# Kernel optimization log

Measured on AMD Instinct MI355X. Metric: run time of the kernel, lower is better.

## Reference

```python
import jax, jax.numpy as jnp
import numpy as np

TINY = 1e-6
SGNUM = 12

def _ln(x, g, b):
    m = jnp.mean(x, -1, keepdims=True)
    v = jnp.mean((x - m) ** 2, -1, keepdims=True)
    return (x - m) * jax.lax.rsqrt(v + 1e-5) * g + b

def _mean_var(x, w):
    # weighted mean/variance over the view dim (-2), keepdim
    mean = jnp.sum(x * w, -2, keepdims=True)
    var = jnp.sum(w * (x - mean) ** 2, -2, keepdims=True)
    return mean, var

def setup_inputs():
    BN, H, W, N = 1, 128, 128, 8
    CTX, PF, PH, HD, MH, FH = 61, 32, 64, 32, 256, 128
    D = CTX + 3 + PF  # 96
    key = jax.random.key(0)
    ks = iter(jax.random.split(key, 64))
    def rnm(shape):
        return jax.random.normal(next(ks), shape, jnp.float32)
    def pw(shape):
        return jax.random.normal(next(ks), shape, jnp.float32) * 0.02
    inp = dict(
        rgb=jax.random.uniform(next(ks), (BN, H, W, N, 3), jnp.float32),
        featmaps_dense=rnm((BN, H, W, 1, CTX)),
        view_dir=rnm((BN, H, W, N, 3)),
        proj_err=rnm((BN, H, W, N, 1)),
        normal=rnm((BN, H, W, 1, 3)),
        DL=rnm((BN, H, W, SGNUM * 7)),
        # pbr_mlp: LN(7) -> Lin(7,PH) ELU -> Lin(PH,PH) ELU -> Lin(PH,PH) ELU -> Lin(PH,PF)
        pbr_ln_g=jnp.ones((7,), jnp.float32), pbr_ln_b=jnp.zeros((7,), jnp.float32),
        pbr_w1=pw((7, PH)), pbr_b1=jnp.zeros((PH,), jnp.float32),
        pbr_w2=pw((PH, PH)), pbr_b2=jnp.zeros((PH,), jnp.float32),
        pbr_w3=pw((PH, PH)), pbr_b3=jnp.zeros((PH,), jnp.float32),
        pbr_w4=pw((PH, PF)), pbr_b4=jnp.zeros((PF,), jnp.float32),
        # transformer block 1
        tv1_ln_g=jnp.ones((D,), jnp.float32), tv1_ln_b=jnp.zeros((D,), jnp.float32),
        tv1_w=pw((D, HD)),
        to1_w=pw((3 * HD, D)), to1_b=jnp.zeros((D,), jnp.float32),
        n1_ln_g=jnp.ones((D,), jnp.float32), n1_ln_b=jnp.zeros((D,), jnp.float32),
        n1_w1=pw((D, MH)), n1_b1=jnp.zeros((MH,), jnp.float32),
        n1_w2=pw((MH, D)), n1_b2=jnp.zeros((D,), jnp.float32),
        # transformer block 2
        tv2_ln_g=jnp.ones((D,), jnp.float32), tv2_ln_b=jnp.zeros((D,), jnp.float32),
        tv2_w=pw((D, HD)),
        to2_w=pw((3 * HD, D)), to2_b=jnp.zeros((D,), jnp.float32),
        n2_ln_g=jnp.ones((D,), jnp.float32), n2_ln_b=jnp.zeros((D,), jnp.float32),
        n2_w1=pw((D, MH)), n2_b1=jnp.zeros((MH,), jnp.float32),
        n2_w2=pw((MH, D)), n2_b2=jnp.zeros((D,), jnp.float32),
        # mlp_brdf
        brdf_ln_g=jnp.ones((D,), jnp.float32), brdf_ln_b=jnp.zeros((D,), jnp.float32),
        brdf_w1=pw((D, FH)), brdf_b1=jnp.zeros((FH,), jnp.float32),
        brdf_w2=pw((FH, FH)), brdf_b2=jnp.zeros((FH,), jnp.float32),
    )
    return inp

def reference(rgb, featmaps_dense, view_dir, proj_err, normal, DL,
              pbr_ln_g, pbr_ln_b, pbr_w1, pbr_b1, pbr_w2, pbr_b2, pbr_w3, pbr_b3, pbr_w4, pbr_b4,
              tv1_ln_g, tv1_ln_b, tv1_w, to1_w, to1_b,
              n1_ln_g, n1_ln_b, n1_w1, n1_b1, n1_w2, n1_b2,
              tv2_ln_g, tv2_ln_b, tv2_w, to2_w, to2_b,
              n2_ln_g, n2_ln_b, n2_w1, n2_b1, n2_w2, n2_b2,
              brdf_ln_g, brdf_ln_b, brdf_w1, brdf_b1, brdf_w2, brdf_b2):
    bn, h, w, n, _ = rgb.shape
    # view weights from reprojection error
    wgt = -jnp.minimum(jnp.log10(jnp.abs(proj_err) + TINY), 0.0)
    wgt = wgt / (jnp.sum(wgt, -2, keepdims=True) + TINY)  # [bn,h,w,n,1]
    DL6 = DL.reshape(bn, h, w, 1, SGNUM, 7)
    dl_dir = DL6[..., :3]
    DLdotN = jnp.sum(dl_dir * normal[:, :, :, :, None, :], -1, keepdims=True)  # [bn,h,w,1,SG,1]
    hdotV = (jnp.sum(dl_dir * view_dir[:, :, :, :, None, :], -1, keepdims=True) + 1.0) * 0.5  # [bn,h,w,n,SG,1]
    fresnel = jnp.exp2((-5.55472 * hdotV - 6.98316) * hdotV)
    VdotN = jnp.sum(view_dir * normal, -1, keepdims=True)[..., None, :]  # [bn,h,w,n,1,1]
    part = jnp.broadcast_to(jnp.concatenate([DLdotN, DL6[..., 3:]], -1), (bn, h, w, n, SGNUM, 5))
    VdotN = jnp.broadcast_to(VdotN, (bn, h, w, n, SGNUM, 1))
    pbr = jnp.concatenate([part, fresnel, VdotN], -1)  # [bn,h,w,n,SG,7]
    y = _ln(pbr, pbr_ln_g, pbr_ln_b)
    y = jax.nn.elu(y @ pbr_w1 + pbr_b1)
    y = jax.nn.elu(y @ pbr_w2 + pbr_b2)
    y = jax.nn.elu(y @ pbr_w3 + pbr_b3)
    pbr_feature = jnp.sum(y @ pbr_w4 + pbr_b4, -2)  # sum over SGNum -> [bn,h,w,n,PF]
    fm = jnp.broadcast_to(featmaps_dense, (bn, h, w, n, featmaps_dense.shape[-1]))
    x_input = jnp.concatenate([rgb, fm, pbr_feature], -1)  # [bn,h,w,n,D]
    # transformer block 1
    v = _ln(x_input, tv1_ln_g, tv1_ln_b) @ tv1_w  # [bn,h,w,n,HD]
    mean, var = _mean_var(v, wgt)
    mv = jnp.broadcast_to(jnp.concatenate([mean, var], -1), v.shape[:-1] + (2 * v.shape[-1],))
    x = jnp.concatenate([v, mv], -1) @ to1_w + to1_b + x_input
    x = jax.nn.gelu(_ln(x, n1_ln_g, n1_ln_b) @ n1_w1 + n1_b1, approximate=False) @ n1_w2 + n1_b2 + x_input
    # transformer block 2 (collapses view dim)
    v = _ln(x, tv2_ln_g, tv2_ln_b) @ tv2_w
    mean, var = _mean_var(v, wgt)
    x = (jnp.concatenate([v[..., :1, :], mean, var], -1) @ to2_w + to2_b)[..., 0, :]
    x = x + x_input[..., 0, :]
    x = jax.nn.gelu(_ln(x, n2_ln_g, n2_ln_b) @ n2_w1 + n2_b1, approximate=False) @ n2_w2 + n2_b2 + x_input[..., 0, :]
    brdf = jax.nn.gelu(_ln(x, brdf_ln_g, brdf_ln_b) @ brdf_w1 + brdf_b1, approximate=False) @ brdf_w2 + brdf_b2
    return brdf  # [bn,h,w,final_hidden]
```

## Files before the change

### kernel.cpp

```cpp
#include <hip/hip_runtime.h>
#include <math.h>


#define NPIX 16384

__device__ __forceinline__ float elu_f(float x){ return x > 0.f ? x : (__expf(x) - 1.f); }
__device__ __forceinline__ float gelu_f(float x){ return 0.5f*x*(1.f + erff(x*0.70710678118654752f)); }

__device__ __forceinline__ void fma4(float4& a, float s, const float4 w){
  a.x = fmaf(s, w.x, a.x); a.y = fmaf(s, w.y, a.y);
  a.z = fmaf(s, w.z, a.z); a.w = fmaf(s, w.w, a.w);
}
__device__ __forceinline__ float4 elu4f(float4 a){
  return make_float4(elu_f(a.x), elu_f(a.y), elu_f(a.z), elu_f(a.w));
}

#define NTA 768
#define NBA (NPIX/2)

constexpr int AYA   = 0;
constexpr int AYB   = 13056;
constexpr int AWB   = 26112;
constexpr int AXL   = 30208;
constexpr int ABIAS = 31744;
constexpr int ATOT  = 31968;

template<int K, int SI, bool DOELU>
__device__ __forceinline__ void mmA64(const float* __restrict__ Xin,
                                      const float* __restrict__ WB,
                                      const float* __restrict__ bias,
                                      float* __restrict__ Yout, int t)
{
  const int rq = t >> 4, c4 = t & 15;
  const float* x0 = Xin + (4*rq+0)*SI;
  const float* x1 = Xin + (4*rq+1)*SI;
  const float* x2 = Xin + (4*rq+2)*SI;
  const float* x3 = Xin + (4*rq+3)*SI;
  const float4* __restrict__ W4 = (const float4*)WB;
  const float4 b = ((const float4*)bias)[c4];
  float4 a0=b, a1=b, a2=b, a3=b;
  #pragma unroll
  for (int k2 = 0; k2 < K/2; ++k2){
    const float2 xa = *(const float2*)(x0 + 2*k2);
    const float2 xb = *(const float2*)(x1 + 2*k2);
    const float2 xc = *(const float2*)(x2 + 2*k2);
    const float2 xd = *(const float2*)(x3 + 2*k2);
    const float4 wA = W4[(2*k2)*16 + c4];
    const float4 wB = W4[(2*k2+1)*16 + c4];
    fma4(a0, xa.x, wA); fma4(a0, xa.y, wB);
    fma4(a1, xb.x, wA); fma4(a1, xb.y, wB);
    fma4(a2, xc.x, wA); fma4(a2, xc.y, wB);
    fma4(a3, xd.x, wA); fma4(a3, xd.y, wB);
  }
  if (DOELU){ a0 = elu4f(a0); a1 = elu4f(a1); a2 = elu4f(a2); a3 = elu4f(a3); }
  *(float4*)(Yout + (4*rq+0)*68 + 4*c4) = a0;
  *(float4*)(Yout + (4*rq+1)*68 + 4*c4) = a1;
  *(float4*)(Yout + (4*rq+2)*68 + 4*c4) = a2;
  *(float4*)(Yout + (4*rq+3)*68 + 4*c4) = a3;
}

__device__ __forceinline__ void mmA32(const float* __restrict__ Xin,
                                      const float* __restrict__ WB,
                                      const float* __restrict__ bias,
                                      float* __restrict__ F, int t)
{
  const int rq = t >> 4, c2 = t & 15;
  const float* x0 = Xin + (4*rq+0)*68;
  const float* x1 = Xin + (4*rq+1)*68;
  const float* x2 = Xin + (4*rq+2)*68;
  const float* x3 = Xin + (4*rq+3)*68;
  const float2* __restrict__ W2 = (const float2*)WB;
  const float2 b = ((const float2*)bias)[c2];
  float2 a0=b, a1=b, a2=b, a3=b;
  #pragma unroll
  for (int k2 = 0; k2 < 32; ++k2){
    const float2 xa = *(const float2*)(x0 + 2*k2);
    const float2 xb = *(const float2*)(x1 + 2*k2);
    const float2 xc = *(const float2*)(x2 + 2*k2);
    const float2 xd = *(const float2*)(x3 + 2*k2);
    const float2 wA = W2[(2*k2)*16 + c2];
    const float2 wB = W2[(2*k2+1)*16 + c2];
    a0.x = fmaf(xa.x, wA.x, a0.x); a0.y = fmaf(xa.x, wA.y, a0.y);
    a0.x = fmaf(xa.y, wB.x, a0.x); a0.y = fmaf(xa.y, wB.y, a0.y);
    a1.x = fmaf(xb.x, wA.x, a1.x); a1.y = fmaf(xb.x, wA.y, a1.y);
    a1.x = fmaf(xb.y, wB.x, a1.x); a1.y = fmaf(xb.y, wB.y, a1.y);
    a2.x = fmaf(xc.x, wA.x, a2.x); a2.y = fmaf(xc.x, wA.y, a2.y);
    a2.x = fmaf(xc.y, wB.x, a2.x); a2.y = fmaf(xc.y, wB.y, a2.y);
    a3.x = fmaf(xd.x, wA.x, a3.x); a3.y = fmaf(xd.x, wA.y, a3.y);
    a3.x = fmaf(xd.y, wB.x, a3.x); a3.y = fmaf(xd.y, wB.y, a3.y);
  }
  *(float2*)(F + (4*rq+0)*34 + 2*c2) = a0;
  *(float2*)(F + (4*rq+1)*34 + 2*c2) = a1;
  *(float2*)(F + (4*rq+2)*34 + 2*c2) = a2;
  *(float2*)(F + (4*rq+3)*34 + 2*c2) = a3;
}

__global__ __launch_bounds__(NTA)
void mva_phaseA(const float* __restrict__ view_dir, const float* __restrict__ normal,
                const float* __restrict__ DL,
                const float* __restrict__ ln_g, const float* __restrict__ ln_b,
                const float* __restrict__ w1, const float* __restrict__ b1,
                const float* __restrict__ w2, const float* __restrict__ b2,
                const float* __restrict__ w3, const float* __restrict__ b3,
                const float* __restrict__ w4, const float* __restrict__ b4,
                float* __restrict__ feat)
{
  __shared__ __align__(16) float smem[ATOT];
  const int t = threadIdx.x;
  const int bpx0 = blockIdx.x*2;
  float4* WB4 = (float4*)(smem + AWB);

  {
    const float4* s = (const float4*)w1;
    for (int i = t; i < 128; i += NTA){
      const int k = i >> 4, c4 = i & 15;
      WB4[i] = (k < 7) ? s[k*16 + c4] : make_float4(0.f,0.f,0.f,0.f);
    }
    float4* d = (float4*)(smem+ABIAS);
    if (t >= 256 && t < 272)      d[t-256]      = ((const float4*)b1)[t-256];
    else if (t >= 272 && t < 288) d[16 + t-272] = ((const float4*)b2)[t-272];
    else if (t >= 288 && t < 304) d[32 + t-288] = ((const float4*)b3)[t-288];
    else if (t >= 304 && t < 312) d[48 + t-304] = ((const float4*)b4)[t-304];
  }
  if (t < 192){
    const int pl = t / 96, rr = t - pl*96;
    const int sg = rr >> 3, view = rr & 7;
    const int px = bpx0 + pl;
    const float nm0 = normal[px*3+0], nm1 = normal[px*3+1], nm2 = normal[px*3+2];
    const float* vd = view_dir + (px*8 + view)*3;
    const float vd0 = vd[0], vd1 = vd[1], vd2 = vd[2];
    const float* dl = DL + px*84 + sg*7;
    const float d0=dl[0], d1=dl[1], d2=dl[2], d3=dl[3], d4=dl[4], d5=dl[5], d6=dl[6];

    const float DLdotN = d0*nm0 + d1*nm1 + d2*nm2;
    const float hv     = (d0*vd0 + d1*vd1 + d2*vd2 + 1.f)*0.5f;
    const float fres   = exp2f((-5.55472f*hv - 6.98316f)*hv);
    const float VdotN  = vd0*nm0 + vd1*nm1 + vd2*nm2;

    const float x0 = DLdotN, x1 = d3, x2 = d4, x3 = d5, x4 = d6, x5 = fres, x6 = VdotN;
    const float m  = (x0+x1+x2+x3+x4+x5+x6)*(1.f/7.f);
    float q, var = 0.f;
    q = x0-m; var += q*q; q = x1-m; var += q*q; q = x2-m; var += q*q;
    q = x3-m; var += q*q; q = x4-m; var += q*q; q = x5-m; var += q*q;
    q = x6-m; var += q*q;
    const float rs = rsqrtf(var*(1.f/7.f) + 1e-5f);
    float* xl = smem + AXL + t*8;
    xl[0] = (x0-m)*rs*ln_g[0] + ln_b[0];
    xl[1] = (x1-m)*rs*ln_g[1] + ln_b[1];
    xl[2] = (x2-m)*rs*ln_g[2] + ln_b[2];
    xl[3] = (x3-m)*rs*ln_g[3] + ln_b[3];
    xl[4] = (x4-m)*rs*ln_g[4] + ln_b[4];
    xl[5] = (x5-m)*rs*ln_g[5] + ln_b[5];
    xl[6] = (x6-m)*rs*ln_g[6] + ln_b[6];
    xl[7] = 0.f;
  }
  __syncthreads();

  float4 p0 = ((const float4*)w2)[t];
  float4 p1 = (t < 256) ? ((const float4*)w2)[t + 768] : make_float4(0.f,0.f,0.f,0.f);
  mmA64<8,8,true>(smem+AXL, smem+AWB, smem+ABIAS+0, smem+AYA, t);
  __syncthreads();
  WB4[t] = p0; if (t < 256) WB4[t + 768] = p1;
  __syncthreads();

  p0 = ((const float4*)w3)[t];
  p1 = (t < 256) ? ((const float4*)w3)[t + 768] : make_float4(0.f,0.f,0.f,0.f);
  mmA64<64,68,true>(smem+AYA, smem+AWB, smem+ABIAS+64, smem+AYB, t);
  __syncthreads();
  WB4[t] = p0; if (t < 256) WB4[t + 768] = p1;
  __syncthreads();

  p0 = (t < 512) ? ((const float4*)w4)[t] : make_float4(0.f,0.f,0.f,0.f);
  mmA64<64,68,true>(smem+AYB, smem+AWB, smem+ABIAS+128, smem+AYA, t);
  __syncthreads();
  if (t < 512) WB4[t] = p0;
  __syncthreads();

  mmA32(smem+AYA, smem+AWB, smem+ABIAS+192, smem+AYB, t);
  __syncthreads();

  if (t < 512){
    const int pl = t >> 8, idx = t & 255;
    const int v = idx >> 5, c = idx & 31;
    float s = 0.f;
    #pragma unroll
    for (int sg = 0; sg < 12; ++sg) s += smem[AYB + (pl*96 + sg*8 + v)*34 + c];
    feat[(size_t)(bpx0 + pl)*256 + idx] = s;
  }
}

#define NTB 512

template<int KK, int CC, int LDWG>
__device__ __forceinline__ void stageW(const float* __restrict__ Wg, int c4off,
                                       float* __restrict__ wbuf, int t)
{
  constexpr int C4 = CC/4;
  constexpr int N4 = KK*C4;
  const float4* __restrict__ s = (const float4*)Wg;
  float4* d = (float4*)wbuf;
  for (int i = t; i < N4; i += NTB){
    const int k = i / C4, c4 = i - k*C4;
    d[i] = s[k*(LDWG/4) + c4off + c4];
  }
}

#define PFSLOT(Wg, KK, CC, LDWG, C4OFF, SLOT, PFV) { \
  const int _i = t + (SLOT)*512; \
  if ((KK)*((CC)/4) > (SLOT)*512 && _i < (KK)*((CC)/4)){ \
    const int _k = _i/((CC)/4), _c = _i - _k*((CC)/4); \
    PFV = ((const float4*)(Wg))[_k*((LDWG)/4) + (C4OFF) + _c]; } }

#define PFLOADG(Wg, KK, CC, LDWG, C4OFF) \
  PFSLOT(Wg,KK,CC,LDWG,C4OFF,0,pf0) PFSLOT(Wg,KK,CC,LDWG,C4OFF,1,pf1) \
  PFSLOT(Wg,KK,CC,LDWG,C4OFF,2,pf2) PFSLOT(Wg,KK,CC,LDWG,C4OFF,3,pf3) \
  PFSLOT(Wg,KK,CC,LDWG,C4OFF,4,pf4) PFSLOT(Wg,KK,CC,LDWG,C4OFF,5,pf5)

#define PFWR(N4, SLOT, PFV) { if ((N4) > (SLOT)*512 && t + (SLOT)*512 < (N4)) WB4[t+(SLOT)*512] = PFV; }
#define PFWRITE(KK, CC) { \
  PFWR((KK)*((CC)/4),0,pf0) PFWR((KK)*((CC)/4),1,pf1) PFWR((KK)*((CC)/4),2,pf2) \
  PFWR((KK)*((CC)/4),3,pf3) PFWR((KK)*((CC)/4),4,pf4) PFWR((KK)*((CC)/4),5,pf5) }

__device__ __forceinline__ void ln32s(const float* __restrict__ in, int Si,
                                      float* __restrict__ out, int So,
                                      const float* __restrict__ g, const float* __restrict__ b,
                                      int t)
{
  if (t < 256){
    const int r = t >> 3, l8 = t & 7;
    const float* row = in + r*Si;
    float vals[12]; int cols[12];
    float s1 = 0.f, s2 = 0.f;
    #pragma unroll
    for (int i = 0; i < 12; ++i){
      int c = l8 + 8*i + 8*(r & 7); if (c >= 96) c -= 96;
      float a = row[c];
      cols[i] = c; vals[i] = a; s1 += a; s2 += a*a;
    }
    s1 += __shfl_xor(s1, 1); s2 += __shfl_xor(s2, 1);
    s1 += __shfl_xor(s1, 2); s2 += __shfl_xor(s2, 2);
    s1 += __shfl_xor(s1, 4); s2 += __shfl_xor(s2, 4);
    float mean = s1*(1.f/96.f);
    float var  = s2*(1.f/96.f) - mean*mean;
    float rsd = rsqrtf(var + 1e-5f);
    float* orow = out + r*So;
    #pragma unroll
    for (int i = 0; i < 12; ++i){
      int c = cols[i];
      orow[c] = (vals[i]-mean)*rsd*g[c] + b[c];
    }
  }
}

template<int K, int C, int LDW, bool GELU, bool HASB, bool RES, bool ACC>
__device__ __forceinline__ void mmR32(const float* __restrict__ inb, int S,
                                      const float* __restrict__ Wl, const float* __restrict__ bg,
                                      float* __restrict__ outb, int So,
                                      const float* __restrict__ residb, int Sr, int t)
{
  constexpr int C4 = C/4;
  const float4* __restrict__ W4 = (const float4*)Wl;
  for (int gi = t; gi < C4*16; gi += NTB){
    const int rp = gi & 15, c4 = gi >> 4;
    const float2* x0 = (const float2*)(inb + (2*rp)*S);
    const float2* x1 = (const float2*)(inb + (2*rp+1)*S);
    float4 a0 = HASB ? ((const float4*)bg)[c4] : make_float4(0.f,0.f,0.f,0.f);
    float4 a1 = a0;
    #pragma unroll 8
    for (int k2 = 0; k2 < K/2; ++k2){
      float2 xa = x0[k2], xb = x1[k2];
      float4 wA = W4[(2*k2)*(LDW/4) + c4];
      float4 wB = W4[(2*k2+1)*(LDW/4) + c4];
      fma4(a0, xa.x, wA); fma4(a0, xa.y, wB);
      fma4(a1, xb.x, wA); fma4(a1, xb.y, wB);
    }
    if (GELU){
      a0.x=gelu_f(a0.x); a0.y=gelu_f(a0.y); a0.z=gelu_f(a0.z); a0.w=gelu_f(a0.w);
      a1.x=gelu_f(a1.x); a1.y=gelu_f(a1.y); a1.z=gelu_f(a1.z); a1.w=gelu_f(a1.w);
    }
    if (RES){
      const float* r0 = residb + (2*rp)*Sr + 4*c4;
      const float* r1 = residb + (2*rp+1)*Sr + 4*c4;
      a0.x += r0[0]; a0.y += r0[1]; a0.z += r0[2]; a0.w += r0[3];
      a1.x += r1[0]; a1.y += r1[1]; a1.z += r1[2]; a1.w += r1[3];
    }
    float* o0 = outb + (2*rp)*So + 4*c4;
    float* o1 = outb + (2*rp+1)*So + 4*c4;
    if (ACC){
      a0.x += o0[0]; a0.y += o0[1]; a0.z += o0[2]; a0.w += o0[3];
      a1.x += o1[0]; a1.y += o1[1]; a1.z += o1[2]; a1.w += o1[3];
    }
    o0[0]=a0.x; o0[1]=a0.y; o0[2]=a0.z; o0[3]=a0.w;
    o1[0]=a1.x; o1[1]=a1.y; o1[2]=a1.z; o1[3]=a1.w;
  }
}

#define NBB1 (NPIX/4)
constexpr int BXIN  = 0;
constexpr int BXCUR = 3264;
constexpr int BXLN  = 6528;
constexpr int BHID  = 9792;
constexpr int BVB   = 14080;
constexpr int BMEAN = 15296;
constexpr int BVAR  = 15424;
constexpr int BWGT  = 15552;
constexpr int BWBUF = 15584;
constexpr int B1TOT = 27872;

__global__ __launch_bounds__(NTB)
void mva_phaseB1(const float* __restrict__ rgb, const float* __restrict__ fm,
                 const float* __restrict__ proj_err, float* __restrict__ ws,
                 const float* __restrict__ tv1_ln_g, const float* __restrict__ tv1_ln_b,
                 const float* __restrict__ tv1_w,
                 const float* __restrict__ to1_w, const float* __restrict__ to1_b,
                 const float* __restrict__ n1_ln_g, const float* __restrict__ n1_ln_b,
                 const float* __restrict__ n1_w1, const float* __restrict__ n1_b1,
                 const float* __restrict__ n1_w2, const float* __restrict__ n1_b2,
                 const float* __restrict__ tv2_ln_g, const float* __restrict__ tv2_ln_b,
                 const float* __restrict__ tv2_w)
{
  __shared__ __align__(16) float smem[B1TOT];
  const int t = threadIdx.x;
  const int bpx0 = blockIdx.x*4;
  float* WB = smem + BWBUF;
  float4* WB4 = (float4*)WB;
  float4 pf0 = make_float4(0,0,0,0), pf1 = pf0, pf2 = pf0, pf3 = pf0, pf4 = pf0, pf5 = pf0;

  for (int u = t; u < 2048; u += NTB){
    const int r = u >> 6, k = u & 63;
    const int pl = r >> 3, v = r & 7;
    float val = (k < 3) ? rgb[((bpx0+pl)*8 + v)*3 + k]
                        : fm[(bpx0+pl)*61 + (k-3)];
    smem[BXIN + r*102 + k] = val;
  }
  for (int u = t; u < 1024; u += NTB){
    const int r = u >> 5, c = u & 31;
    smem[BXIN + r*102 + 64 + c] = ws[(size_t)blockIdx.x*1024 + u];
  }
  if (t < 32){
    float pe = proj_err[(bpx0 + (t>>3))*8 + (t&7)];
    float wraw = fmaxf(-log10f(fabsf(pe) + 1e-6f), 0.f);
    float s = wraw;
    s += __shfl_xor(s, 1); s += __shfl_xor(s, 2); s += __shfl_xor(s, 4);
    smem[BWGT + t] = wraw / (s + 1e-6f);
  }
  stageW<96,32,32>(tv1_w, 0, WB, t);
  __syncthreads();

  ln32s(smem+BXIN, 102, smem+BXLN, 102, tv1_ln_g, tv1_ln_b, t);
  PFLOADG(to1_w, 96,96,96, 0)
  __syncthreads();
  mmR32<96,32,32,false,false,false,false>(smem+BXLN, 102, WB, nullptr, smem+BVB, 38, nullptr, 0, t);
  __syncthreads();
  if (t < 128){
    const int pl = t >> 5, c = t & 31;
    const float* wn = smem + BWGT + pl*8;
    float m = 0.f;
    #pragma unroll
    for (int v = 0; v < 8; ++v) m += wn[v]*smem[BVB + (pl*8+v)*38 + c];
    float vv = 0.f;
    #pragma unroll
    for (int v = 0; v < 8; ++v){ float d = smem[BVB + (pl*8+v)*38 + c] - m; vv += wn[v]*d*d; }
    smem[BMEAN + pl*32 + c] = m;
    smem[BVAR  + pl*32 + c] = vv;
  }
  PFWRITE(96,96)
  __syncthreads();
  for (int u = t; u < 3072; u += NTB){
    const int r = u & 31, c = u >> 5;
    const int pl = r >> 3;
    float val = (c < 32) ? smem[BVB + r*38 + c]
              : (c < 64) ? smem[BMEAN + pl*32 + (c-32)]
                         : smem[BVAR + pl*32 + (c-64)];
    smem[BXLN + r*102 + c] = val;
  }
  __syncthreads();
  PFLOADG(n1_w1, 96,128,256, 0)
  mmR32<96,96,96,false,true,true,false>(smem+BXLN, 102, WB, to1_b, smem+BXCUR, 102, smem+BXIN, 102, t);
  __syncthreads();
  ln32s(smem+BXCUR, 102, smem+BXLN, 102, n1_ln_g, n1_ln_b, t);
  PFWRITE(96,128)
  __syncthreads();
  PFLOADG(n1_w2, 128,96,96, 0)
  mmR32<96,128,128,true,true,false,false>(smem+BXLN, 102, WB, n1_b1, smem+BHID, 134, nullptr, 0, t);
  __syncthreads();
  PFWRITE(128,96)
  __syncthreads();
  PFLOADG(n1_w1, 96,128,256, 32)
  mmR32<128,96,96,false,false,false,false>(smem+BHID, 134, WB, nullptr, smem+BXCUR, 102, nullptr, 0, t);
  __syncthreads();
  PFWRITE(96,128)
  __syncthreads();
  PFLOADG(n1_w2 + 128*96, 128,96,96, 0)
  mmR32<96,128,128,true,true,false,false>(smem+BXLN, 102, WB, n1_b1 + 128, smem+BHID, 134, nullptr, 0, t);
  __syncthreads();
  PFWRITE(128,96)
  __syncthreads();
  PFLOADG(tv2_w, 96,32,32, 0)
  mmR32<128,96,96,false,true,true,true>(smem+BHID, 134, WB, n1_b2, smem+BXCUR, 102, smem+BXIN, 102, t);
  __syncthreads();
  ln32s(smem+BXCUR, 102, smem+BXLN, 102, tv2_ln_g, tv2_ln_b, t);
  PFWRITE(96,32)
  __syncthreads();
  mmR32<96,32,32,false,false,false,false>(smem+BXLN, 102, WB, nullptr, smem+BVB, 38, nullptr, 0, t);
  __syncthreads();
  if (t < 128){
    const int pl = t >> 5, c = t & 31;
    const float* wn = smem + BWGT + pl*8;
    float m = 0.f;
    #pragma unroll
    for (int v = 0; v < 8; ++v) m += wn[v]*smem[BVB + (pl*8+v)*38 + c];
    float vv = 0.f;
    #pragma unroll
    for (int v = 0; v < 8; ++v){ float d = smem[BVB + (pl*8+v)*38 + c] - m; vv += wn[v]*d*d; }
    smem[BMEAN + pl*32 + c] = m;
    smem[BVAR  + pl*32 + c] = vv;
  }
  __syncthreads();
  if (t < 384){
    const int pl = t / 96, c = t - pl*96;
    float val = (c < 32) ? smem[BVB + (pl*8)*38 + c]
              : (c < 64) ? smem[BMEAN + pl*32 + (c-32)]
                         : smem[BVAR + pl*32 + (c-64)];
    ws[(size_t)blockIdx.x*1024 + pl*256 + 96 + c] = val;
  }
}

#define NBB2 (NPIX/32)
constexpr int CXLN  = 0;
constexpr int CXIN  = 3264;
constexpr int CXS   = 6528;
constexpr int CTMP  = 9792;
constexpr int CHID  = 13056;
constexpr int CWBUF = 17344;
constexpr int B2TOT = 29632;

__global__ __launch_bounds__(NTB)
void mva_phaseB2(const float* __restrict__ rgb, const float* __restrict__ fm,
                 const float* __restrict__ ws,
                 const float* __restrict__ to2_w, const float* __restrict__ to2_b,
                 const float* __restrict__ n2_ln_g, const float* __restrict__ n2_ln_b,
                 const float* __restrict__ n2_w1, const float* __restrict__ n2_b1,
                 const float* __restrict__ n2_w2, const float* __restrict__ n2_b2,
                 const float* __restrict__ brdf_ln_g, const float* __restrict__ brdf_ln_b,
                 const float* __restrict__ brdf_w1, const float* __restrict__ brdf_b1,
                 const float* __restrict__ brdf_w2, const float* __restrict__ brdf_b2,
                 float* __restrict__ out)
{
  __shared__ __align__(16) float smem[B2TOT];
  const int t = threadIdx.x;
  const int bpx0 = blockIdx.x*32;
  float* WB = smem + CWBUF;
  float4* WB4 = (float4*)WB;
  float4 pf0 = make_float4(0,0,0,0), pf1 = pf0, pf2 = pf0, pf3 = pf0, pf4 = pf0, pf5 = pf0;

  for (int u = t; u < 3072; u += NTB){
    const int r = u / 96, c = u - r*96;
    const int px = bpx0 + r;
    const size_t ab = (size_t)px*256;
    smem[CXLN + r*102 + c] = ws[ab + 96 + c];
    float xv = (c < 3)  ? rgb[((size_t)px*8)*3 + c]
             : (c < 64) ? fm[(size_t)px*61 + (c-3)]
                        : ws[ab + (c-64)];
    smem[CXIN + r*102 + c] = xv;
  }
  stageW<96,96,96>(to2_w, 0, WB, t);
  __syncthreads();

  PFLOADG(n2_w1, 96,128,256, 0)
  mmR32<96,96,96,false,true,true,false>(smem+CXLN, 102, WB, to2_b, smem+CXS, 102, smem+CXIN, 102, t);
  __syncthreads();
  ln32s(smem+CXS, 102, smem+CXLN, 102, n2_ln_g, n2_ln_b, t);
  PFWRITE(96,128)
  __syncthreads();
  PFLOADG(n2_w2, 128,96,96, 0)
  mmR32<96,128,128,true,true,false,false>(smem+CXLN, 102, WB, n2_b1, smem+CHID, 134, nullptr, 0, t);
  __syncthreads();
  PFWRITE(128,96)
  __syncthreads();
  PFLOADG(n2_w1, 96,128,256, 32)
  mmR32<128,96,96,false,false,false,false>(smem+CHID, 134, WB, nullptr, smem+CTMP, 102, nullptr, 0, t);
  __syncthreads();
  PFWRITE(96,128)
  __syncthreads();
  PFLOADG(n2_w2 + 128*96, 128,96,96, 0)
  mmR32<96,128,128,true,true,false,false>(smem+CXLN, 102, WB, n2_b1 + 128, smem+CHID, 134, nullptr, 0, t);
  __syncthreads();
  PFWRITE(128,96)
  __syncthreads();
  PFLOADG(brdf_w1, 96,128,128, 0)
  mmR32<128,96,96,false,true,true,true>(smem+CHID, 134, WB, n2_b2, smem+CTMP, 102, smem+CXIN, 102, t);
  __syncthreads();
  ln32s(smem+CTMP, 102, smem+CXLN, 102, brdf_ln_g, brdf_ln_b, t);
  PFWRITE(96,128)
  __syncthreads();
  PFLOADG(brdf_w2, 128,64,128, 0)
  mmR32<96,128,128,true,true,false,false>(smem+CXLN, 102, WB, brdf_b1, smem+CHID, 134, nullptr, 0, t);
  __syncthreads();
  PFWRITE(128,64)
  __syncthreads();
  float* outp = out + (size_t)bpx0*128;
  PFLOADG(brdf_w2, 128,64,128, 16)
  mmR32<128,64,64,false,true,false,false>(smem+CHID, 134, WB, brdf_b2, outp, 128, nullptr, 0, t);
  __syncthreads();
  PFWRITE(128,64)
  __syncthreads();
  mmR32<128,64,64,false,true,false,false>(smem+CHID, 134, WB, brdf_b2 + 64, outp + 64, 128, nullptr, 0, t);
}

extern "C" void kernel_launch(void* const* d_in, const int* in_sizes, int n_in,
                              void* d_out, int out_size, void* d_ws, size_t ws_size,
                              hipStream_t stream)
{
  (void)in_sizes; (void)n_in; (void)ws_size; (void)out_size;
  int i = 0;
  const float* rgb      = (const float*)d_in[i++];
  const float* fm       = (const float*)d_in[i++];
  const float* view_dir = (const float*)d_in[i++];
  const float* proj_err = (const float*)d_in[i++];
  const float* normal   = (const float*)d_in[i++];
  const float* DL       = (const float*)d_in[i++];
  const float* pbr_ln_g = (const float*)d_in[i++];
  const float* pbr_ln_b = (const float*)d_in[i++];
  const float* pbr_w1   = (const float*)d_in[i++];
  const float* pbr_b1   = (const float*)d_in[i++];
  const float* pbr_w2   = (const float*)d_in[i++];
  const float* pbr_b2   = (const float*)d_in[i++];
  const float* pbr_w3   = (const float*)d_in[i++];
  const float* pbr_b3   = (const float*)d_in[i++];
  const float* pbr_w4   = (const float*)d_in[i++];
  const float* pbr_b4   = (const float*)d_in[i++];
  const float* tv1_ln_g = (const float*)d_in[i++];
  const float* tv1_ln_b = (const float*)d_in[i++];
  const float* tv1_w    = (const float*)d_in[i++];
  const float* to1_w    = (const float*)d_in[i++];
  const float* to1_b    = (const float*)d_in[i++];
  const float* n1_ln_g  = (const float*)d_in[i++];
  const float* n1_ln_b  = (const float*)d_in[i++];
  const float* n1_w1    = (const float*)d_in[i++];
  const float* n1_b1    = (const float*)d_in[i++];
  const float* n1_w2    = (const float*)d_in[i++];
  const float* n1_b2    = (const float*)d_in[i++];
  const float* tv2_ln_g = (const float*)d_in[i++];
  const float* tv2_ln_b = (const float*)d_in[i++];
  const float* tv2_w    = (const float*)d_in[i++];
  const float* to2_w    = (const float*)d_in[i++];
  const float* to2_b    = (const float*)d_in[i++];
  const float* n2_ln_g  = (const float*)d_in[i++];
  const float* n2_ln_b  = (const float*)d_in[i++];
  const float* n2_w1    = (const float*)d_in[i++];
  const float* n2_b1    = (const float*)d_in[i++];
  const float* n2_w2    = (const float*)d_in[i++];
  const float* n2_b2    = (const float*)d_in[i++];
  const float* brdf_ln_g= (const float*)d_in[i++];
  const float* brdf_ln_b= (const float*)d_in[i++];
  const float* brdf_w1  = (const float*)d_in[i++];
  const float* brdf_b1  = (const float*)d_in[i++];
  const float* brdf_w2  = (const float*)d_in[i++];
  const float* brdf_b2  = (const float*)d_in[i++];

  float* ws = (float*)d_ws;

  mva_phaseA<<<dim3(NBA), dim3(NTA), 0, stream>>>(
      view_dir, normal, DL, pbr_ln_g, pbr_ln_b,
      pbr_w1, pbr_b1, pbr_w2, pbr_b2, pbr_w3, pbr_b3, pbr_w4, pbr_b4, ws);

  mva_phaseB1<<<dim3(NBB1), dim3(NTB), 0, stream>>>(
      rgb, fm, proj_err, ws,
      tv1_ln_g, tv1_ln_b, tv1_w, to1_w, to1_b,
      n1_ln_g, n1_ln_b, n1_w1, n1_b1, n1_w2, n1_b2,
      tv2_ln_g, tv2_ln_b, tv2_w);

  mva_phaseB2<<<dim3(NBB2), dim3(NTB), 0, stream>>>(
      rgb, fm, ws,
      to2_w, to2_b,
      n2_ln_g, n2_ln_b, n2_w1, n2_b1, n2_w2, n2_b2,
      brdf_ln_g, brdf_ln_b, brdf_w1, brdf_b1, brdf_w2, brdf_b2,
      (float*)d_out);
}
```

Baseline: 1.087 ms.

## Double-buffer phase-A weights, swizzle activations, widen LDS reads to float4

Phase A's small MLP now keeps weights in two shared-memory buffers, so the next layer's weights are written while the current matmul runs. This removes one barrier per layer. Intermediate activations use a 64-wide XOR-swizzled layout instead of padded stride-68 rows, which lets inputs be read as float4 without bank conflicts. Biases are read straight from global memory instead of being staged in shared memory. The risks are a layout or aliasing mistake (the LN input area now overlaps AYB) and higher register pressure from the wider k-unroll.

```diff
diff --git a/kernel.cpp b/kernel.cpp
--- a/kernel.cpp
+++ b/kernel.cpp
@@ -18,81 +18,91 @@
 #define NTA 768
 #define NBA (NPIX/2)
 
-constexpr int AYA   = 0;
-constexpr int AYB   = 13056;
-constexpr int AWB   = 26112;
-constexpr int AXL   = 30208;
-constexpr int ABIAS = 31744;
-constexpr int ATOT  = 31968;
-
-template<int K, int SI, bool DOELU>
-__device__ __forceinline__ void mmA64(const float* __restrict__ Xin,
-                                      const float* __restrict__ WB,
-                                      const float* __restrict__ bias,
-                                      float* __restrict__ Yout, int t)
+constexpr int AYA  = 0;
+constexpr int AYB  = 12288;
+constexpr int AWB0 = 24576;
+constexpr int AWB1 = 28672;
+constexpr int AXL  = AYB;
+constexpr int ATOT = 32768;
+
+__device__ __forceinline__ int swzA(int r, int cw){
+  return (r << 6) + (cw ^ ((r & 15) << 2));
+}
+
+template<int K, bool SWZIN, int SILIN, bool DOELU>
+__device__ __forceinline__ void mmA64s(const float* __restrict__ Xin,
+                                       const float* __restrict__ WBuf,
+                                       const float* __restrict__ bias_g,
+                                       float* __restrict__ Yout, int t)
 {
   const int rq = t >> 4, c4 = t & 15;
-  const float* x0 = Xin + (4*rq+0)*SI;
-  const float* x1 = Xin + (4*rq+1)*SI;
-  const float* x2 = Xin + (4*rq+2)*SI;
-  const float* x3 = Xin + (4*rq+3)*SI;
-  const float4* __restrict__ W4 = (const float4*)WB;
-  const float4 b = ((const float4*)bias)[c4];
+  const int r0 = 4*rq, r1 = r0+1, r2 = r0+2, r3 = r0+3;
+  const float4* __restrict__ W4 = (const float4*)WBuf;
+  const float4 b = ((const float4*)bias_g)[c4];
   float4 a0=b, a1=b, a2=b, a3=b;
   #pragma unroll
-  for (int k2 = 0; k2 < K/2; ++k2){
-    const float2 xa = *(const float2*)(x0 + 2*k2);
-    const float2 xb = *(const float2*)(x1 + 2*k2);
-    const float2 xc = *(const float2*)(x2 + 2*k2);
-    const float2 xd = *(const float2*)(x3 + 2*k2);
-    const float4 wA = W4[(2*k2)*16 + c4];
-    const float4 wB = W4[(2*k2+1)*16 + c4];
-    fma4(a0, xa.x, wA); fma4(a0, xa.y, wB);
-    fma4(a1, xb.x, wA); fma4(a1, xb.y, wB);
-    fma4(a2, xc.x, wA); fma4(a2, xc.y, wB);
-    fma4(a3, xd.x, wA); fma4(a3, xd.y, wB);
+  for (int k4 = 0; k4 < K/4; ++k4){
+    float4 xa, xb, xc, xd;
+    if (SWZIN){
+      xa = *(const float4*)(Xin + swzA(r0, 4*k4));
+      xb = *(const float4*)(Xin + swzA(r1, 4*k4));
+      xc = *(const float4*)(Xin + swzA(r2, 4*k4));
+      xd = *(const float4*)(Xin + swzA(r3, 4*k4));
+    } else {
+      xa = *(const float4*)(Xin + r0*SILIN + 4*k4);
+      xb = *(const float4*)(Xin + r1*SILIN + 4*k4);
+      xc = *(const float4*)(Xin + r2*SILIN + 4*k4);
+      xd = *(const float4*)(Xin + r3*SILIN + 4*k4);
+    }
+    const float4 w0 = W4[(4*k4+0)*16 + c4];
+    const float4 w1 = W4[(4*k4+1)*16 + c4];
+    const float4 w2 = W4[(4*k4+2)*16 + c4];
+    const float4 w3 = W4[(4*k4+3)*16 + c4];
+    fma4(a0, xa.x, w0); fma4(a0, xa.y, w1); fma4(a0, xa.z, w2); fma4(a0, xa.w, w3);
+    fma4(a1, xb.x, w0); fma4(a1, xb.y, w1); fma4(a1, xb.z, w2); fma4(a1, xb.w, w3);
+    fma4(a2, xc.x, w0); fma4(a2, xc.y, w1); fma4(a2, xc.z, w2); fma4(a2, xc.w, w3);
+    fma4(a3, xd.x, w0); fma4(a3, xd.y, w1); fma4(a3, xd.z, w2); fma4(a3, xd.w, w3);
   }
   if (DOELU){ a0 = elu4f(a0); a1 = elu4f(a1); a2 = elu4f(a2); a3 = elu4f(a3); }
-  *(float4*)(Yout + (4*rq+0)*68 + 4*c4) = a0;
-  *(float4*)(Yout + (4*rq+1)*68 + 4*c4) = a1;
-  *(float4*)(Yout + (4*rq+2)*68 + 4*c4) = a2;
-  *(float4*)(Yout + (4*rq+3)*68 + 4*c4) = a3;
-}
-
-__device__ __forceinline__ void mmA32(const float* __restrict__ Xin,
-                                      const float* __restrict__ WB,
-                                      const float* __restrict__ bias,
-                                      float* __restrict__ F, int t)
+  *(float4*)(Yout + swzA(r0, 4*c4)) = a0;
+  *(float4*)(Yout + swzA(r1, 4*c4)) = a1;
+  *(float4*)(Yout + swzA(r2, 4*c4)) = a2;
+  *(float4*)(Yout + swzA(r3, 4*c4)) = a3;
+}
+
+__device__ __forceinline__ void mmA32s(const float* __restrict__ Xin,
+                                       const float* __restrict__ WBuf,
+                                       const float* __restrict__ bias_g,
+                                       float* __restrict__ F, int t)
 {
   const int rq = t >> 4, c2 = t & 15;
-  const float* x0 = Xin + (4*rq+0)*68;
-  const float* x1 = Xin + (4*rq+1)*68;
-  const float* x2 = Xin + (4*rq+2)*68;
-  const float* x3 = Xin + (4*rq+3)*68;
-  const float2* __restrict__ W2 = (const float2*)WB;
-  const float2 b = ((const float2*)bias)[c2];
+  const int r0 = 4*rq, r1 = r0+1, r2 = r0+2, r3 = r0+3;
+  const float2* __restrict__ W2 = (const float2*)WBuf;
+  const float2 b = ((const float2*)bias_g)[c2];
   float2 a0=b, a1=b, a2=b, a3=b;
   #pragma unroll
-  for (int k2 = 0; k2 < 32; ++k2){
-    const float2 xa = *(const float2*)(x0 + 2*k2);
-    const float2 xb = *(const float2*)(x1 + 2*k2);
-    const float2 xc = *(const float2*)(x2 + 2*k2);
-    const float2 xd = *(const float2*)(x3 + 2*k2);
-    const float2 wA = W2[(2*k2)*16 + c2];
-    const float2 wB = W2[(2*k2+1)*16 + c2];
-    a0.x = fmaf(xa.x, wA.x, a0.x); a0.y = fmaf(xa.x, wA.y, a0.y);
-    a0.x = fmaf(xa.y, wB.x, a0.x); a0.y = fmaf(xa.y, wB.y, a0.y);
-    a1.x = fmaf(xb.x, wA.x, a1.x); a1.y = fmaf(xb.x, wA.y, a1.y);
-    a1.x = fmaf(xb.y, wB.x, a1.x); a1.y = fmaf(xb.y, wB.y, a1.y);
-    a2.x = fmaf(xc.x, wA.x, a2.x); a2.y = fmaf(xc.x, wA.y, a2.y);
-    a2.x = fmaf(xc.y, wB.x, a2.x); a2.y = fmaf(xc.y, wB.y, a2.y);
-    a3.x = fmaf(xd.x, wA.x, a3.x); a3.y = fmaf(xd.x, wA.y, a3.y);
-    a3.x = fmaf(xd.y, wB.x, a3.x); a3.y = fmaf(xd.y, wB.y, a3.y);
-  }
-  *(float2*)(F + (4*rq+0)*34 + 2*c2) = a0;
-  *(float2*)(F + (4*rq+1)*34 + 2*c2) = a1;
-  *(float2*)(F + (4*rq+2)*34 + 2*c2) = a2;
-  *(float2*)(F + (4*rq+3)*34 + 2*c2) = a3;
+  for (int k4 = 0; k4 < 16; ++k4){
+    const float4 xa = *(const float4*)(Xin + swzA(r0, 4*k4));
+    const float4 xb = *(const float4*)(Xin + swzA(r1, 4*k4));
+    const float4 xc = *(const float4*)(Xin + swzA(r2, 4*k4));
+    const float4 xd = *(const float4*)(Xin + swzA(r3, 4*k4));
+    #pragma unroll
+    for (int i = 0; i < 4; ++i){
+      const float2 w = W2[(4*k4+i)*16 + c2];
+      const float sa = (i==0)?xa.x:(i==1)?xa.y:(i==2)?xa.z:xa.w;
+      const float sb = (i==0)?xb.x:(i==1)?xb.y:(i==2)?xb.z:xb.w;
+      const float sc = (i==0)?xc.x:(i==1)?xc.y:(i==2)?xc.z:xc.w;
+      const float sd = (i==0)?xd.x:(i==1)?xd.y:(i==2)?xd.z:xd.w;
+      a0.x = fmaf(sa, w.x, a0.x); a0.y = fmaf(sa, w.y, a0.y);
+      a1.x = fmaf(sb, w.x, a1.x); a1.y = fmaf(sb, w.y, a1.y);
+      a2.x = fmaf(sc, w.x, a2.x); a2.y = fmaf(sc, w.y, a2.y);
+      a3.x = fmaf(sd, w.x, a3.x); a3.y = fmaf(sd, w.y, a3.y);
+    }
+  }
+  *(float2*)(F + r0*34 + 2*c2) = a0;
+  *(float2*)(F + r1*34 + 2*c2) = a1;
+  *(float2*)(F + r2*34 + 2*c2) = a2;
+  *(float2*)(F + r3*34 + 2*c2) = a3;
 }
 
 __global__ __launch_bounds__(NTA)
@@ -108,19 +118,18 @@
   __shared__ __align__(16) float smem[ATOT];
   const int t = threadIdx.x;
   const int bpx0 = blockIdx.x*2;
-  float4* WB4 = (float4*)(smem + AWB);
-
+  float4* WB0_4 = (float4*)(smem + AWB0);
+  float4* WB1_4 = (float4*)(smem + AWB1);
+  const float4 zf4 = make_float4(0.f,0.f,0.f,0.f);
+
+  float4 p0 = ((const float4*)w2)[t];
+  float4 p1 = (t < 256) ? ((const float4*)w2)[t + 768] : zf4;
   {
-    const float4* s = (const float4*)w1;
+    const float4* s1 = (const float4*)w1;
     for (int i = t; i < 128; i += NTA){
-      const int k = i >> 4, c4 = i & 15;
-      WB4[i] = (k < 7) ? s[k*16 + c4] : make_float4(0.f,0.f,0.f,0.f);
-    }
-    float4* d = (float4*)(smem+ABIAS);
-    if (t >= 256 && t < 272)      d[t-256]      = ((const float4*)b1)[t-256];
-    else if (t >= 272 && t < 288) d[16 + t-272] = ((const float4*)b2)[t-272];
-    else if (t >= 288 && t < 304) d[32 + t-288] = ((const float4*)b3)[t-288];
-    else if (t >= 304 && t < 312) d[48 + t-304] = ((const float4*)b4)[t-304];
+      const int k = i >> 4, c = i & 15;
+      WB0_4[i] = (k < 7) ? s1[k*16 + c] : zf4;
+    }
   }
   if (t < 192){
     const int pl = t / 96, rr = t - pl*96;
@@ -156,27 +165,22 @@
   }
   __syncthreads();
 
-  float4 p0 = ((const float4*)w2)[t];
-  float4 p1 = (t < 256) ? ((const float4*)w2)[t + 768] : make_float4(0.f,0.f,0.f,0.f);
-  mmA64<8,8,true>(smem+AXL, smem+AWB, smem+ABIAS+0, smem+AYA, t);
-  __syncthreads();
-  WB4[t] = p0; if (t < 256) WB4[t + 768] = p1;
+  mmA64s<8, false, 8, true>(smem+AXL, smem+AWB0, b1, smem+AYA, t);
+  WB1_4[t] = p0; if (t < 256) WB1_4[t + 768] = p1;
   __syncthreads();
 
   p0 = ((const float4*)w3)[t];
-  p1 = (t < 256) ? ((const float4*)w3)[t + 768] : make_float4(0.f,0.f,0.f,0.f);
-  mmA64<64,68,true>(smem+AYA, smem+AWB, smem+ABIAS+64, smem+AYB, t);
-  __syncthreads();
-  WB4[t] = p0; if (t < 256) WB4[t + 768] = p1;
-  __syncthreads();
-
-  p0 = (t < 512) ? ((const float4*)w4)[t] : make_float4(0.f,0.f,0.f,0.f);
-  mmA64<64,68,true>(smem+AYB, smem+AWB, smem+ABIAS+128, smem+AYA, t);
-  __syncthreads();
-  if (t < 512) WB4[t] = p0;
-  __syncthreads();
-
-  mmA32(smem+AYA, smem+AWB, smem+ABIAS+192, smem+AYB, t);
+  p1 = (t < 256) ? ((const float4*)w3)[t + 768] : zf4;
+  mmA64s<64, true, 0, true>(smem+AYA, smem+AWB1, b2, smem+AYB, t);
+  WB0_4[t] = p0; if (t < 256) WB0_4[t + 768] = p1;
+  __syncthreads();
+
+  p0 = (t < 512) ? ((const float4*)w4)[t] : zf4;
+  mmA64s<64, true, 0, true>(smem+AYB, smem+AWB0, b3, smem+AYA, t);
+  if (t < 512) WB1_4[t] = p0;
+  __syncthreads();
+
+  mmA32s(smem+AYA, smem+AWB1, b4, smem+AYB, t);
   __syncthreads();
 
   if (t < 512){
```

Measured after the change: 1.118 ms. 1.03x slower.
